# Kernel tuning notes

Hardware: AMD Instinct MI355X
Metric: run time of the kernel (lower is better)

Reference implementation:

```python
import jax, jax.numpy as jnp
import numpy as np

B, N, D_IN, D_HID, D_EDGE = 4, 256, 256, 256, 64


def setup_inputs() -> dict:
    key = jax.random.key(0)
    ks = jax.random.split(key, 8)
    s_in = 1.0 / np.sqrt(D_IN)
    s_h2 = 1.0 / np.sqrt(2 * D_HID)
    s_h = 1.0 / np.sqrt(D_HID)
    return {
        "x": jax.random.normal(ks[0], (B, N, D_IN), jnp.float32),
        "W_in": jax.random.uniform(ks[1], (D_HID, D_IN), jnp.float32, -s_in, s_in),
        "b_in": jax.random.uniform(ks[2], (D_HID,), jnp.float32, -s_in, s_in),
        "W1": jax.random.uniform(ks[3], (D_HID, 2 * D_HID), jnp.float32, -s_h2, s_h2),
        "b1": jax.random.uniform(ks[4], (D_HID,), jnp.float32, -s_h2, s_h2),
        "W2": jax.random.uniform(ks[5], (D_EDGE, D_HID), jnp.float32, -s_h, s_h),
        "b2": jax.random.uniform(ks[6], (D_EDGE,), jnp.float32, -s_h, s_h),
    }


def reference(x, W_in, b_in, W1, b1, W2, b2):
    # in_proj: [B,N,d_in] -> [B,N,h]
    h = jnp.einsum("bnd,hd->bnh", x, W_in) + b_in
    # cat([h_i, h_j]) @ W1 == h_i @ Wa + h_j @ Wb with W1 = [Wa | Wb].
    # Precompute the two N x h projections, then broadcast-add over the pair grid
    # instead of materializing the [B,N,N,2h] concat (same math, fused form).
    Wa, Wb = W1[:, :D_HID], W1[:, D_HID:]
    pa = jnp.einsum("bnh,gh->bng", h, Wa)  # [B,N,h]
    pb = jnp.einsum("bnh,gh->bng", h, Wb)  # [B,N,h]
    z = pa[:, :, None, :] + pb[:, None, :, :] + b1  # [B,N,N,h]
    z = z * jax.nn.sigmoid(z)  # Swish
    return jnp.einsum("bijh,eh->bije", z, W2) + b2  # [B,N,N,d_edge]
```

## Files before the change

kernel.cpp:

```cpp
#include <hip/hip_runtime.h>

#define DIN 256
#define DHID 256
#define DEDGE 64
#define BS 136
#define BS2 72

typedef float f32x4 __attribute__((ext_vector_type(4)));
typedef short s16x8 __attribute__((ext_vector_type(8)));
typedef unsigned int u32x2 __attribute__((ext_vector_type(2)));
typedef unsigned int u32x4 __attribute__((ext_vector_type(4)));

__device__ __forceinline__ unsigned int cvtpk(float lo, float hi) {
    unsigned int r;
    asm("v_cvt_pk_bf16_f32 %0, %1, %2" : "=v"(r) : "v"(lo), "v"(hi));
    return r;
}

__device__ __forceinline__ void split4(const f32x4 v, u32x2& hi, u32x2& lo) {
    const unsigned int h0 = cvtpk(v[0], v[1]), h1 = cvtpk(v[2], v[3]);
    f32x4 hf;
    hf[0] = __builtin_bit_cast(float, h0 << 16);
    hf[1] = __builtin_bit_cast(float, h0 & 0xffff0000u);
    hf[2] = __builtin_bit_cast(float, h1 << 16);
    hf[3] = __builtin_bit_cast(float, h1 & 0xffff0000u);
    const f32x4 l = v - hf;
    hi = (u32x2){h0, h1};
    lo = (u32x2){cvtpk(l[0], l[1]), cvtpk(l[2], l[3])};
}

__global__ __launch_bounds__(256) void k_xh(
    const float* __restrict__ x, const float* __restrict__ Win,
    float* __restrict__ hp, const float* __restrict__ W2, s16x8* __restrict__ W2f)
{
    const int tid = threadIdx.x;
    if (blockIdx.z == 4) {
        if (tid < 32) {
            const int f = (((blockIdx.x << 2) + blockIdx.y) << 5) + tid;
            const int l15f = f & 15, qf = (f >> 4) & 3, ebf = (f >> 6) & 3, k0f = f >> 8;
            const int row = (ebf << 4) + l15f;
            const int col = (k0f << 5) + (qf << 3);
            const f32x4 w0 = *reinterpret_cast<const f32x4*>(&W2[row * DHID + col]);
            const f32x4 w1 = *reinterpret_cast<const f32x4*>(&W2[row * DHID + col + 4]);
            u32x4 wp;
            wp[0] = cvtpk(w0[0], w0[1]); wp[1] = cvtpk(w0[2], w0[3]);
            wp[2] = cvtpk(w1[0], w1[1]); wp[3] = cvtpk(w1[2], w1[3]);
            W2f[f] = __builtin_bit_cast(s16x8, wp);
        }
        return;
    }

    __shared__ unsigned short Ahi[64 * BS2], Alo[64 * BS2];
    __shared__ unsigned short Bhi[64 * BS2], Blo[64 * BS2];
    const int m0 = blockIdx.x << 6, n0 = blockIdx.y << 6, k0 = blockIdx.z << 6;

    const int srow = tid >> 2, sc0 = (tid & 3) << 2;
    {
        const float* xA = x + (m0 + srow) * DIN + k0 + sc0;
        const float* wB = Win + (n0 + srow) * DIN + k0 + sc0;
#pragma unroll
        for (int g2 = 0; g2 < 4; ++g2) {
            const int c = g2 << 4;
            const int la = srow * BS2 + sc0 + c;
            u32x2 hi, lo;
            split4(*reinterpret_cast<const f32x4*>(xA + c), hi, lo);
            *reinterpret_cast<u32x2*>(&Ahi[la]) = hi;
            *reinterpret_cast<u32x2*>(&Alo[la]) = lo;
            split4(*reinterpret_cast<const f32x4*>(wB + c), hi, lo);
            *reinterpret_cast<u32x2*>(&Bhi[la]) = hi;
            *reinterpret_cast<u32x2*>(&Blo[la]) = lo;
        }
    }
    __syncthreads();

    const int lane = tid & 63, wave = tid >> 6, quad = lane >> 4, l15 = lane & 15;
    const int arow = (wave << 4) + l15;

    f32x4 acc[4];
#pragma unroll
    for (int nb = 0; nb < 4; ++nb) acc[nb] = (f32x4){0.f, 0.f, 0.f, 0.f};

#pragma unroll
    for (int ks = 0; ks < 2; ++ks) {
        const int kcol = (ks << 5) + (quad << 3);
        const s16x8 ahi = *reinterpret_cast<const s16x8*>(&Ahi[arow * BS2 + kcol]);
        const s16x8 alo = *reinterpret_cast<const s16x8*>(&Alo[arow * BS2 + kcol]);
#pragma unroll
        for (int nb = 0; nb < 4; ++nb) {
            const int brow = (nb << 4) + l15;
            const s16x8 bhi = *reinterpret_cast<const s16x8*>(&Bhi[brow * BS2 + kcol]);
            const s16x8 blo = *reinterpret_cast<const s16x8*>(&Blo[brow * BS2 + kcol]);
            acc[nb] = __builtin_amdgcn_mfma_f32_16x16x32_bf16(ahi, bhi, acc[nb], 0, 0, 0);
            acc[nb] = __builtin_amdgcn_mfma_f32_16x16x32_bf16(ahi, blo, acc[nb], 0, 0, 0);
            acc[nb] = __builtin_amdgcn_mfma_f32_16x16x32_bf16(alo, bhi, acc[nb], 0, 0, 0);
        }
    }

    float* dst = hp + ((size_t)blockIdx.z << 18);
    const int mrow = m0 + (wave << 4) + (quad << 2);
#pragma unroll
    for (int nb = 0; nb < 4; ++nb)
#pragma unroll
        for (int r = 0; r < 4; ++r)
            dst[(mrow + r) * DHID + n0 + (nb << 4) + l15] = acc[nb][r];
}

__global__ __launch_bounds__(256) void k_pab(
    const float* __restrict__ hp, const float* __restrict__ W1,
    const float* __restrict__ bin, float* __restrict__ pap, float* __restrict__ pbp)
{
    __shared__ unsigned short Ahi[64 * BS], Alo[64 * BS];
    __shared__ unsigned short Bhi[64 * BS], Blo[64 * BS];
    const int m0 = blockIdx.x << 6;
    const int half = blockIdx.y >> 2;
    const int n0 = (blockIdx.y & 3) << 6;
    const int kc = blockIdx.z;
    const int tid = threadIdx.x;
    const int k0 = kc << 7;

    const int srow = tid >> 2, sc0 = (tid & 3) << 2;
    {
        const float* hpA = hp + (m0 + srow) * DHID + k0 + sc0;
        const float* w1B = W1 + (n0 + srow) * 512 + (half << 8) + k0 + sc0;
        const float* binp = bin + k0 + sc0;
#pragma unroll
        for (int g2 = 0; g2 < 8; ++g2) {
            const int c = g2 << 4;
            f32x4 av = *reinterpret_cast<const f32x4*>(hpA + c);
            av += *reinterpret_cast<const f32x4*>(hpA + c + (1 << 18));
            av += *reinterpret_cast<const f32x4*>(hpA + c + (2 << 18));
            av += *reinterpret_cast<const f32x4*>(hpA + c + (3 << 18));
            av += *reinterpret_cast<const f32x4*>(binp + c);
            const int la = srow * BS + sc0 + c;
            u32x2 hi, lo;
            split4(av, hi, lo);
            *reinterpret_cast<u32x2*>(&Ahi[la]) = hi;
            *reinterpret_cast<u32x2*>(&Alo[la]) = lo;
            split4(*reinterpret_cast<const f32x4*>(w1B + c), hi, lo);
            *reinterpret_cast<u32x2*>(&Bhi[la]) = hi;
            *reinterpret_cast<u32x2*>(&Blo[la]) = lo;
        }
    }
    __syncthreads();

    const int lane = tid & 63, wave = tid >> 6, quad = lane >> 4, l15 = lane & 15;
    const int arow = (wave << 4) + l15;

    f32x4 acc[4];
#pragma unroll
    for (int nb = 0; nb < 4; ++nb) acc[nb] = (f32x4){0.f, 0.f, 0.f, 0.f};

#pragma unroll
    for (int ks = 0; ks < 4; ++ks) {
        const int kcol = (ks << 5) + (quad << 3);
        const s16x8 ahi = *reinterpret_cast<const s16x8*>(&Ahi[arow * BS + kcol]);
        const s16x8 alo = *reinterpret_cast<const s16x8*>(&Alo[arow * BS + kcol]);
#pragma unroll
        for (int nb = 0; nb < 4; ++nb) {
            const int brow = (nb << 4) + l15;
            const s16x8 bhi = *reinterpret_cast<const s16x8*>(&Bhi[brow * BS + kcol]);
            const s16x8 blo = *reinterpret_cast<const s16x8*>(&Blo[brow * BS + kcol]);
            acc[nb] = __builtin_amdgcn_mfma_f32_16x16x32_bf16(ahi, bhi, acc[nb], 0, 0, 0);
            acc[nb] = __builtin_amdgcn_mfma_f32_16x16x32_bf16(ahi, blo, acc[nb], 0, 0, 0);
            acc[nb] = __builtin_amdgcn_mfma_f32_16x16x32_bf16(alo, bhi, acc[nb], 0, 0, 0);
        }
    }

    float* dst = (half ? pbp : pap) + ((size_t)kc << 18);
    const int mrow = m0 + (wave << 4) + (quad << 2);
#pragma unroll
    for (int nb = 0; nb < 4; ++nb)
#pragma unroll
        for (int r = 0; r < 4; ++r)
            dst[(mrow + r) * DHID + n0 + (nb << 4) + l15] = acc[nb][r];
}

__global__ __launch_bounds__(256, 4) void k_out(
    const float* __restrict__ pap, const float* __restrict__ pbp,
    const float* __restrict__ b1, const s16x8* __restrict__ W2f,
    const float* __restrict__ b2, float* __restrict__ out)
{
    __shared__ s16x8 w2s[2048];
    __shared__ float pab1[4][DHID];

    const int jb = blockIdx.x, i0 = blockIdx.y << 2, b = blockIdx.z;
    const int tid = threadIdx.x;

    {
        const float b1v = b1[tid];
#pragma unroll
        for (int ii = 0; ii < 4; ++ii) {
            const int off = (((b << 8) + i0 + ii) << 8) + tid;
            pab1[ii][tid] = pap[off] + pap[off + (1 << 18)] + b1v;
        }
    }
#pragma unroll
    for (int it = 0; it < 8; ++it)
        w2s[tid + (it << 8)] = W2f[tid + (it << 8)];
    __syncthreads();

    const int lane = tid & 63, wave = tid >> 6, quad = lane >> 4, l15 = lane & 15;
    const int j0 = (jb << 6) + (wave << 4);
    const int pboff = (((b << 8) + (j0 + l15)) << 8);
    const float* pbq0 = pbp + pboff;
    const float* pbq1 = pbp + (1 << 18) + pboff;

    f32x4 acc[4][4];
#pragma unroll
    for (int ii = 0; ii < 4; ++ii)
#pragma unroll
        for (int eb = 0; eb < 4; ++eb) acc[ii][eb] = (f32x4){0.f, 0.f, 0.f, 0.f};

    float b2v[4];
#pragma unroll
    for (int eb = 0; eb < 4; ++eb) b2v[eb] = b2[(eb << 4) + l15];

#pragma unroll
    for (int k0 = 0; k0 < 8; ++k0) {
        const int g = (k0 << 5) + (quad << 3);
        const f32x4 p0 = *reinterpret_cast<const f32x4*>(pbq0 + g)
                       + *reinterpret_cast<const f32x4*>(pbq1 + g);
        const f32x4 p1 = *reinterpret_cast<const f32x4*>(pbq0 + g + 4)
                       + *reinterpret_cast<const f32x4*>(pbq1 + g + 4);

        s16x8 bfrag[4];
#pragma unroll
        for (int eb = 0; eb < 4; ++eb)
            bfrag[eb] = w2s[((k0 << 2) + eb) * 64 + lane];

#pragma unroll
        for (int ii = 0; ii < 4; ++ii) {
            const f32x4 q0 = *reinterpret_cast<const f32x4*>(&pab1[ii][g]);
            const f32x4 q1 = *reinterpret_cast<const f32x4*>(&pab1[ii][g + 4]);
            float s[8];
#pragma unroll
            for (int jj = 0; jj < 4; ++jj) {
                const float z0 = q0[jj] + p0[jj];
                const float z1 = q1[jj] + p1[jj];
                const float e0 = __expf(-z0);
                const float e1 = __expf(-z1);
                s[jj]     = z0 * __builtin_amdgcn_rcpf(1.0f + e0);
                s[4 + jj] = z1 * __builtin_amdgcn_rcpf(1.0f + e1);
            }
            u32x4 ap;
            ap[0] = cvtpk(s[0], s[1]); ap[1] = cvtpk(s[2], s[3]);
            ap[2] = cvtpk(s[4], s[5]); ap[3] = cvtpk(s[6], s[7]);
            const s16x8 a = __builtin_bit_cast(s16x8, ap);
#pragma unroll
            for (int eb = 0; eb < 4; ++eb)
                acc[ii][eb] = __builtin_amdgcn_mfma_f32_16x16x32_bf16(a, bfrag[eb], acc[ii][eb], 0, 0, 0);
        }
    }

#pragma unroll
    for (int ii = 0; ii < 4; ++ii) {
        const int obase = (((((b << 8) + i0 + ii) << 8) + j0 + (quad << 2)) << 6) + l15;
#pragma unroll
        for (int eb = 0; eb < 4; ++eb) {
#pragma unroll
            for (int r = 0; r < 4; ++r)
                out[obase + (r << 6) + (eb << 4)] = acc[ii][eb][r] + b2v[eb];
        }
    }
}

extern "C" void kernel_launch(void* const* d_in, const int* in_sizes, int n_in,
                              void* d_out, int out_size, void* d_ws, size_t ws_size,
                              hipStream_t stream) {
    const float* x = 0; const float* Win = 0; const float* bin = 0;
    const float* W1 = 0; const float* b1 = 0; const float* W2 = 0; const float* b2 = 0;
    for (int idx = 0; idx < n_in; ++idx) {
        const int s = in_sizes[idx];
        if (s == 262144) x = (const float*)d_in[idx];
        else if (s == 131072) W1 = (const float*)d_in[idx];
        else if (s == 65536) Win = (const float*)d_in[idx];
        else if (s == 16384) W2 = (const float*)d_in[idx];
        else if (s == 64) b2 = (const float*)d_in[idx];
        else if (s == 256) { if (!bin) bin = (const float*)d_in[idx]; else b1 = (const float*)d_in[idx]; }
    }

    float* ws  = (float*)d_ws;
    float* hp  = ws;
    float* pap = hp + (4 << 18);
    float* pbp = pap + (2 << 18);
    float* w2f = pbp + (2 << 18);

    hipLaunchKernelGGL(k_xh,  dim3(16, 4, 5), dim3(256), 0, stream, x, Win, hp, W2, (s16x8*)w2f);
    hipLaunchKernelGGL(k_pab, dim3(16, 8, 2), dim3(256), 0, stream, hp, W1, bin, pap, pbp);
    hipLaunchKernelGGL(k_out, dim3(4, 64, 4), dim3(256), 0, stream,
                       pap, pbp, b1, (const s16x8*)w2f, b2, (float*)d_out);
}
```

Measured before the change: 127.5 us.

## Pre-sum and transpose pb into a new buffer, prefetch it in output kernel

Adds a transpose kernel that sums the two K-split partials of pb and writes them as [b][g][j]. The output kernel reads this transposed buffer, so lanes with consecutive j load coalesced scalars instead of strided float4 pairs from two partial buffers. It also software-prefetches the next k-slice's pb values into registers. The output kernel drops its occupancy hint. The cost is an extra kernel launch and an extra pass over pb through global memory.

Result: faster. 116.8 us (-8.4%).

```diff
diff --git a/kernel.cpp b/kernel.cpp
--- a/kernel.cpp
+++ b/kernel.cpp
@@ -175,8 +175,33 @@
             dst[(mrow + r) * DHID + n0 + (nb << 4) + l15] = acc[nb][r];
 }
 
-__global__ __launch_bounds__(256, 4) void k_out(
-    const float* __restrict__ pap, const float* __restrict__ pbp,
+__global__ __launch_bounds__(256) void k_tr(
+    const float* __restrict__ pbp, float* __restrict__ pbT)
+{
+    __shared__ float t[32][36];
+    const int jt = blockIdx.x << 5, gt = blockIdx.y << 5, b = blockIdx.z;
+    const int tid = threadIdx.x;
+
+    const int jj = tid >> 3, gg = (tid & 7) << 2;
+    {
+        const float* src = pbp + (((b << 8) + jt + jj) << 8) + gt + gg;
+        const f32x4 v = *reinterpret_cast<const f32x4*>(src)
+                      + *reinterpret_cast<const f32x4*>(src + (1 << 18));
+        *reinterpret_cast<f32x4*>(&t[jj][gg]) = v;
+    }
+    __syncthreads();
+
+    const int gg2 = tid >> 3, jj2 = (tid & 7) << 2;
+    {
+        f32x4 v;
+#pragma unroll
+        for (int k = 0; k < 4; ++k) v[k] = t[jj2 + k][gg2];
+        *reinterpret_cast<f32x4*>(&pbT[(b << 16) + ((gt + gg2) << 8) + jt + jj2]) = v;
+    }
+}
+
+__global__ __launch_bounds__(256) void k_out(
+    const float* __restrict__ pap, const float* __restrict__ pbT,
     const float* __restrict__ b1, const s16x8* __restrict__ W2f,
     const float* __restrict__ b2, float* __restrict__ out)
 {
@@ -201,9 +226,7 @@
 
     const int lane = tid & 63, wave = tid >> 6, quad = lane >> 4, l15 = lane & 15;
     const int j0 = (jb << 6) + (wave << 4);
-    const int pboff = (((b << 8) + (j0 + l15)) << 8);
-    const float* pbq0 = pbp + pboff;
-    const float* pbq1 = pbp + (1 << 18) + pboff;
+    const float* pbL = pbT + (b << 16) + j0 + l15;
 
     f32x4 acc[4][4];
 #pragma unroll
@@ -215,13 +238,24 @@
 #pragma unroll
     for (int eb = 0; eb < 4; ++eb) b2v[eb] = b2[(eb << 4) + l15];
 
-#pragma unroll
+    const int gq = quad << 3;
+    f32x4 np0, np1;
+    {
+        const float* a = pbL + (gq << 8);
+#pragma unroll
+        for (int c = 0; c < 4; ++c) { np0[c] = a[c << 8]; np1[c] = a[(c + 4) << 8]; }
+    }
+
     for (int k0 = 0; k0 < 8; ++k0) {
-        const int g = (k0 << 5) + (quad << 3);
-        const f32x4 p0 = *reinterpret_cast<const f32x4*>(pbq0 + g)
-                       + *reinterpret_cast<const f32x4*>(pbq1 + g);
-        const f32x4 p1 = *reinterpret_cast<const f32x4*>(pbq0 + g + 4)
-                       + *reinterpret_cast<const f32x4*>(pbq1 + g + 4);
+        const int g = (k0 << 5) + gq;
+        const f32x4 p0 = np0;
+        const f32x4 p1 = np1;
+        {
+            const int gn = (((k0 + 1) & 7) << 5) + gq;
+            const float* a = pbL + (gn << 8);
+#pragma unroll
+            for (int c = 0; c < 4; ++c) { np0[c] = a[c << 8]; np1[c] = a[(c + 4) << 8]; }
+        }
 
         s16x8 bfrag[4];
 #pragma unroll
@@ -284,9 +318,11 @@
     float* pap = hp + (4 << 18);
     float* pbp = pap + (2 << 18);
     float* w2f = pbp + (2 << 18);
+    float* pbT = w2f + 8192;
 
     hipLaunchKernelGGL(k_xh,  dim3(16, 4, 5), dim3(256), 0, stream, x, Win, hp, W2, (s16x8*)w2f);
     hipLaunchKernelGGL(k_pab, dim3(16, 8, 2), dim3(256), 0, stream, hp, W1, bin, pap, pbp);
+    hipLaunchKernelGGL(k_tr,  dim3(8, 8, 4),  dim3(256), 0, stream, pbp, pbT);
     hipLaunchKernelGGL(k_out, dim3(4, 64, 4), dim3(256), 0, stream,
-                       pap, pbp, b1, (const s16x8*)w2f, b2, (float*)d_out);
-}
+                       pap, pbT, b1, (const s16x8*)w2f, b2, (float*)d_out);
+}
```
